# Performance work log

Hardware: AMD Instinct MI355X
Metric: run time of the kernel (lower is better)

## Reference

```python
import jax, jax.numpy as jnp
import numpy as np

N_EMBD = 1024
N_EXPERTS = 8
TOP_K = 2
D_FF = 4 * N_EMBD


def setup_inputs() -> dict:
    key = jax.random.key(0)
    ks = jax.random.split(key, 6)
    B, S = 4, 2048
    s = 1.0 / np.sqrt(N_EMBD)
    sf = 1.0 / np.sqrt(D_FF)
    x = jax.random.normal(ks[0], (B, S, N_EMBD), dtype=jnp.float32)
    router_w = jax.random.uniform(ks[1], (N_EMBD, N_EXPERTS), minval=-s, maxval=s, dtype=jnp.float32)
    wfc = jax.random.uniform(ks[2], (N_EXPERTS, N_EMBD, D_FF), minval=-s, maxval=s, dtype=jnp.float32)
    bfc = jax.random.uniform(ks[3], (N_EXPERTS, D_FF), minval=-s, maxval=s, dtype=jnp.float32)
    wproj = jax.random.uniform(ks[4], (N_EXPERTS, D_FF, N_EMBD), minval=-sf, maxval=sf, dtype=jnp.float32)
    bproj = jax.random.uniform(ks[5], (N_EXPERTS, N_EMBD), minval=-sf, maxval=sf, dtype=jnp.float32)
    return {"x": x, "router_w": router_w, "wfc": wfc, "bfc": bfc, "wproj": wproj, "bproj": bproj}


def reference(x, router_w, wfc, bfc, wproj, bproj):
    B, S, D = x.shape
    E = wfc.shape[0]
    xf = x.reshape(-1, D)  # [N, D] tokens
    logits = xf @ router_w  # [N, E]
    probs = jax.nn.softmax(logits.astype(jnp.float32), axis=-1)
    w, sel = jax.lax.top_k(probs, TOP_K)  # [N, K]
    w = w / jnp.sum(w, axis=-1, keepdims=True)  # norm_topk_prob
    w = w.astype(x.dtype)
    out = jnp.zeros_like(xf)
    for e in range(E):
        # per-token gate for expert e (0 if not routed here) -- same math as
        # gather -> MLP -> weighted scatter-add in the original
        gate = jnp.sum(jnp.where(sel == e, w, jnp.zeros_like(w)), axis=-1)  # [N]
        h = jax.nn.gelu(xf @ wfc[e] + bfc[e], approximate=False)  # [N, 4D]
        y = h @ wproj[e] + bproj[e]  # [N, D]
        out = out + gate[:, None] * y
    return out.reshape(B, S, D)
```

## Files before the change

### kernel.cpp

```cpp
#include <hip/hip_runtime.h>
#include <hip/hip_bf16.h>


#define N_TOK 8192
#define DMODEL 1024
#define NEXP 8
#define DFF 4096
#define CAP 8192
#define MAXW 136

typedef __attribute__((ext_vector_type(8))) short short8;
typedef __attribute__((ext_vector_type(4))) float f32x4;

#define GLOAD_LDS16(g, l)                                              \
  __builtin_amdgcn_global_load_lds(                                    \
      (const __attribute__((address_space(1))) unsigned int*)(g),      \
      (__attribute__((address_space(3))) unsigned int*)(l), 16, 0, 0)

__device__ __forceinline__ unsigned short f2bf(float f) {
  unsigned u = __float_as_uint(f);
  return (unsigned short)((u + 0x7FFFu + ((u >> 16) & 1u)) >> 16);
}

__device__ __forceinline__ float gelu_f(float v) {
  return 0.5f * v * (1.0f + erff(v * 0.70710678118654752f));
}

__global__ void router_k(const float* __restrict__ x, const float* __restrict__ rw,
                         int* __restrict__ cnt, int* __restrict__ tok,
                         float* __restrict__ gate, unsigned short* __restrict__ xb) {
  int lane = threadIdx.x & 63;
  int t = blockIdx.x * 4 + (threadIdx.x >> 6);
  const float* xr = x + (size_t)t * DMODEL;
  unsigned short* xbr = xb + (size_t)t * DMODEL;
  float p[8];
#pragma unroll
  for (int e = 0; e < 8; ++e) p[e] = 0.0f;
#pragma unroll
  for (int j = 0; j < DMODEL / 64; ++j) {
    int i = lane + j * 64;
    float xv = xr[i];
    xbr[i] = f2bf(xv);
    const float4* r = (const float4*)(rw + (size_t)i * 8);
    float4 a = r[0], b = r[1];
    p[0] += xv * a.x; p[1] += xv * a.y; p[2] += xv * a.z; p[3] += xv * a.w;
    p[4] += xv * b.x; p[5] += xv * b.y; p[6] += xv * b.z; p[7] += xv * b.w;
  }
#pragma unroll
  for (int e = 0; e < 8; ++e) {
#pragma unroll
    for (int off = 32; off; off >>= 1) p[e] += __shfl_xor(p[e], off, 64);
  }
  if (lane == 0) {
    int e1 = 0;
#pragma unroll
    for (int e = 1; e < 8; ++e) if (p[e] > p[e1]) e1 = e;
    int e2 = (e1 == 0) ? 1 : 0;
#pragma unroll
    for (int e = 0; e < 8; ++e) if (e != e1 && p[e] > p[e2]) e2 = e;
    float w1 = 1.0f / (1.0f + expf(p[e2] - p[e1]));
    float w2 = 1.0f - w1;
    int s1 = atomicAdd(&cnt[e1], 1);
    tok[e1 * CAP + s1] = t; gate[e1 * CAP + s1] = w1;
    int s2 = atomicAdd(&cnt[e2], 1);
    tok[e2 * CAP + s2] = t; gate[e2 * CAP + s2] = w2;
  }
}

__global__ void prefix_k(const int* __restrict__ cnt, int* __restrict__ off,
                         int* __restrict__ nwork, int* __restrict__ wl) {
  if (threadIdx.x == 0 && blockIdx.x == 0) {
    int s = 0, n = 0;
    for (int e = 0; e < NEXP; ++e) {
      off[e] = s;
      int ntile = (cnt[e] + 127) >> 7;
      for (int mt = 0; mt < ntile; ++mt) wl[n++] = (e << 16) | mt;
      s += cnt[e];
    }
    nwork[0] = n;
  }
}

__global__ __launch_bounds__(256) void cvt_wt_k(const float* __restrict__ W,
                                                unsigned short* __restrict__ WT,
                                                int K, int N) {
  __shared__ float ls[64][68];
  int b = blockIdx.x;
  int nkt = K >> 6, nnt = N >> 6;
  int kt = b % nkt;
  int nt = (b / nkt) % nnt;
  int e = b / (nkt * nnt);
  const float* Wb = W + (size_t)e * K * N + (size_t)(kt * 64) * N + nt * 64;
  int t = threadIdx.x;
  int nn = (t & 15) * 4, kr = t >> 4;
#pragma unroll
  for (int i = 0; i < 4; ++i) {
    float4 v = *(const float4*)(Wb + (size_t)(kr + 16 * i) * N + nn);
    *(float4*)&ls[kr + 16 * i][nn] = v;
  }
  __syncthreads();
  int on = t >> 2, kc = (t & 3) * 16;
  unsigned short* dst = WT + (size_t)e * N * K + (size_t)(nt * 64 + on) * K + kt * 64 + kc;
  short8 r0, r1;
#pragma unroll
  for (int j = 0; j < 8; ++j) r0[j] = (short)f2bf(ls[kc + j][on]);
#pragma unroll
  for (int j = 0; j < 8; ++j) r1[j] = (short)f2bf(ls[kc + 8 + j][on]);
  *(short8*)dst = r0;
  *(short8*)(dst + 8) = r1;
}

#define STAGE(buf, kk)                                                  \
  do {                                                                  \
    GLOAD_LDS16(gA + (kk), &As[buf][tid * 8]);                          \
    GLOAD_LDS16(gB + (kk), &Bs[buf][tid * 8]);                          \
    GLOAD_LDS16(gB2 + (kk), &Bs[buf][4096 + tid * 8]);                  \
  } while (0)

#define COMPUTE(buf)                                                            \
  do {                                                                          \
    short8 af[4], bfv[4];                                                       \
    _Pragma("unroll") for (int i = 0; i < 4; ++i)                               \
        af[i] = *(const short8*)&As[buf][(wr * 64 + i * 16 + fr) * 32 + co];    \
    _Pragma("unroll") for (int i = 0; i < 4; ++i)                               \
        bfv[i] = *(const short8*)&Bs[buf][(wc * 64 + i * 16 + fr) * 32 + co];   \
    _Pragma("unroll") for (int mi = 0; mi < 4; ++mi)                            \
        _Pragma("unroll") for (int ni = 0; ni < 4; ++ni)                        \
            acc[mi][ni] = __builtin_amdgcn_mfma_f32_16x16x32_bf16(              \
                af[mi], bfv[ni], acc[mi][ni], 0, 0, 0);                         \
  } while (0)

#define WAITV(n) asm volatile("s_waitcnt vmcnt(" #n ")" ::: "memory")
#define BAR() __builtin_amdgcn_s_barrier()

#define KLOOP(KTOT)                                                       \
  STAGE(0, 0);                                                            \
  STAGE(1, 32);                                                           \
  STAGE(2, 64);                                                           \
  {                                                                       \
    int k0 = 0;                                                           \
    _Pragma("unroll 1") for (int it = 0; it < ((KTOT) / 32 - 5) / 3; ++it) { \
      WAITV(6); BAR(); COMPUTE(0); BAR(); STAGE(0, k0 + 96);              \
      WAITV(6); BAR(); COMPUTE(1); BAR(); STAGE(1, k0 + 128);             \
      WAITV(6); BAR(); COMPUTE(2); BAR(); STAGE(2, k0 + 160);             \
      k0 += 96;                                                           \
    }                                                                     \
    WAITV(6); BAR(); COMPUTE(0); BAR(); STAGE(0, k0 + 96);                \
    WAITV(6); BAR(); COMPUTE(1); BAR(); STAGE(1, k0 + 128);               \
    WAITV(6); BAR(); COMPUTE(2);                                          \
    WAITV(3); BAR(); COMPUTE(0);                                          \
    WAITV(0); BAR(); COMPUTE(1);                                          \
  }

#define NT1 16
__global__ __launch_bounds__(512, 4) void gemm1a_k(
    const unsigned short* __restrict__ xb, const unsigned short* __restrict__ wT,
    const float* __restrict__ bfc, const int* __restrict__ cnt,
    const int* __restrict__ off, const int* __restrict__ tok,
    const int* __restrict__ nwork, const int* __restrict__ wl,
    unsigned short* __restrict__ h) {
  int bid = (int)(blockIdx.x & 7) * ((int)gridDim.x >> 3) + (int)(blockIdx.x >> 3);
  int widx = bid % MAXW;
  int nt = bid / MAXW;
  if (widx >= nwork[0]) return;
  int wle = wl[widx];
  int e = wle >> 16;
  int mt = wle & 0xffff;
  int Me = cnt[e];
  int base = off[e];
  int n0 = nt * 256;

  __shared__ __align__(16) unsigned short As[3][128 * 32];
  __shared__ __align__(16) unsigned short Bs[3][256 * 32];

  int tid = threadIdx.x;
  int lane = tid & 63, w = tid >> 6;
  int lc = (((tid & 3) ^ ((tid >> 2) & 3)) * 8);

  int ari = mt * 128 + (tid >> 2);
  int t0 = tok[e * CAP + ((ari < Me) ? ari : (Me - 1))];
  const unsigned short* gA = xb + (size_t)t0 * DMODEL + lc;
  const unsigned short* gB = wT + ((size_t)e * DFF + n0 + (tid >> 2)) * DMODEL + lc;
  const unsigned short* gB2 = gB + (size_t)128 * DMODEL;

  int wr = w >> 2, wc = w & 3;
  int g = lane >> 4, fr = lane & 15;
  int co = ((g ^ (fr & 3)) * 8);

  f32x4 acc[4][4];
#pragma unroll
  for (int i = 0; i < 4; ++i)
#pragma unroll
    for (int j = 0; j < 4; ++j) acc[i][j] = (f32x4)0.0f;

  KLOOP(DMODEL);

#pragma unroll
  for (int mi = 0; mi < 4; ++mi) {
    int rl = wr * 64 + mi * 16 + g * 4;
#pragma unroll
    for (int i = 0; i < 4; ++i) {
      int r = mt * 128 + rl + i;
      if (r < Me) {
        unsigned short* hrow = h + (size_t)(base + r) * DFF;
#pragma unroll
        for (int ni = 0; ni < 4; ++ni) {
          int col = n0 + wc * 64 + ni * 16 + fr;
          float v = acc[mi][ni][i] + bfc[e * DFF + col];
          hrow[col] = f2bf(gelu_f(v));
        }
      }
    }
  }
}

#define NT2 4
__global__ __launch_bounds__(512, 4) void gemm2a_k(
    const unsigned short* __restrict__ h, const unsigned short* __restrict__ wT,
    const float* __restrict__ bproj, const int* __restrict__ cnt,
    const int* __restrict__ off, const int* __restrict__ tok,
    const int* __restrict__ nwork, const int* __restrict__ wl,
    const float* __restrict__ gate, float* __restrict__ out) {
  int bid = (int)(blockIdx.x & 7) * ((int)gridDim.x >> 3) + (int)(blockIdx.x >> 3);
  int widx = bid % MAXW;
  int nt = bid / MAXW;
  if (widx >= nwork[0]) return;
  int wle = wl[widx];
  int e = wle >> 16;
  int mt = wle & 0xffff;
  int Me = cnt[e];
  int base = off[e];
  int n0 = nt * 256;

  __shared__ __align__(16) unsigned short As[3][128 * 32];
  __shared__ __align__(16) unsigned short Bs[3][256 * 32];

  int tid = threadIdx.x;
  int lane = tid & 63, w = tid >> 6;
  int lc = (((tid & 3) ^ ((tid >> 2) & 3)) * 8);

  const unsigned short* gA = h + (size_t)(base + mt * 128 + (tid >> 2)) * DFF + lc;
  const unsigned short* gB = wT + ((size_t)e * DMODEL + n0 + (tid >> 2)) * DFF + lc;
  const unsigned short* gB2 = gB + (size_t)128 * DFF;

  int wr = w >> 2, wc = w & 3;
  int g = lane >> 4, fr = lane & 15;
  int co = ((g ^ (fr & 3)) * 8);

  f32x4 acc[4][4];
#pragma unroll
  for (int i = 0; i < 4; ++i)
#pragma unroll
    for (int j = 0; j < 4; ++j) acc[i][j] = (f32x4)0.0f;

  KLOOP(DFF);

#pragma unroll
  for (int mi = 0; mi < 4; ++mi) {
    int rl = wr * 64 + mi * 16 + g * 4;
#pragma unroll
    for (int i = 0; i < 4; ++i) {
      int r = mt * 128 + rl + i;
      if (r < Me) {
        int tkn = tok[e * CAP + r];
        float gv = gate[e * CAP + r];
        float* orow = out + (size_t)tkn * DMODEL;
#pragma unroll
        for (int ni = 0; ni < 4; ++ni) {
          int col = n0 + wc * 64 + ni * 16 + fr;
          float v = acc[mi][ni][i] + bproj[e * DMODEL + col];
          atomicAdd(orow + col, gv * v);
        }
      }
    }
  }
}

extern "C" void kernel_launch(void* const* d_in, const int* in_sizes, int n_in,
                              void* d_out, int out_size, void* d_ws, size_t ws_size,
                              hipStream_t stream) {
  const float* x = (const float*)d_in[0];
  const float* rw = (const float*)d_in[1];
  const float* wfc = (const float*)d_in[2];
  const float* bfc = (const float*)d_in[3];
  const float* wproj = (const float*)d_in[4];
  const float* bproj = (const float*)d_in[5];
  float* out = (float*)d_out;

  char* ws = (char*)d_ws;
  int* cnt = (int*)ws;
  int* off_ = (int*)(ws + 64);
  int* nwork = (int*)(ws + 128);
  int* wl = (int*)(ws + 256);
  int* tok = (int*)(ws + 4096);
  float* gate = (float*)(ws + 4096 + (size_t)NEXP * CAP * 4);
  size_t HOFF = 4096 + 2 * (size_t)NEXP * CAP * 4;
  unsigned short* h = (unsigned short*)(ws + HOFF);
  size_t HSZ = (size_t)(16384 + 128) * DFF * 2;
  size_t XOFF = HOFF + HSZ;
  size_t WOFF = XOFF + (size_t)N_TOK * DMODEL * 2;
  size_t WSZ = (size_t)NEXP * DFF * DMODEL * 2;
  unsigned short* xb = (unsigned short*)(ws + XOFF);
  unsigned short* wT1 = (unsigned short*)(ws + WOFF);

  hipMemsetAsync(cnt, 0, 128, stream);
  hipMemsetAsync(out, 0, (size_t)out_size * 4, stream);
  router_k<<<N_TOK / 4, 256, 0, stream>>>(x, rw, cnt, tok, gate, xb);
  prefix_k<<<1, 64, 0, stream>>>(cnt, off_, nwork, wl);

  if (ws_size >= WOFF + 2 * WSZ) {
    unsigned short* wT2 = (unsigned short*)(ws + WOFF + WSZ);
    cvt_wt_k<<<NEXP * (DMODEL / 64) * (DFF / 64), 256, 0, stream>>>(wfc, wT1, DMODEL, DFF);
    cvt_wt_k<<<NEXP * (DFF / 64) * (DMODEL / 64), 256, 0, stream>>>(wproj, wT2, DFF, DMODEL);
    gemm1a_k<<<MAXW * NT1, 512, 0, stream>>>(xb, wT1, bfc, cnt, off_, tok, nwork, wl, h);
    gemm2a_k<<<MAXW * NT2, 512, 0, stream>>>(h, wT2, bproj, cnt, off_, tok, nwork, wl, gate, out);
  } else {
    cvt_wt_k<<<NEXP * (DMODEL / 64) * (DFF / 64), 256, 0, stream>>>(wfc, wT1, DMODEL, DFF);
    gemm1a_k<<<MAXW * NT1, 512, 0, stream>>>(xb, wT1, bfc, cnt, off_, tok, nwork, wl, h);
    cvt_wt_k<<<NEXP * (DFF / 64) * (DMODEL / 64), 256, 0, stream>>>(wproj, wT1, DFF, DMODEL);
    gemm2a_k<<<MAXW * NT2, 512, 0, stream>>>(h, wT1, bproj, cnt, off_, tok, nwork, wl, gate, out);
  }
}
```

Before: 815.0 us.

## Enlarge GEMM tiles to 256x256x64 with double-buffered LDS and setprio

```diff
diff --git a/kernel.cpp b/kernel.cpp
--- a/kernel.cpp
+++ b/kernel.cpp
@@ -7,7 +7,7 @@
 #define NEXP 8
 #define DFF 4096
 #define CAP 8192
-#define MAXW 136
+#define MAXW 72
 
 typedef __attribute__((ext_vector_type(8))) short short8;
 typedef __attribute__((ext_vector_type(4))) float f32x4;
@@ -73,7 +73,7 @@
     int s = 0, n = 0;
     for (int e = 0; e < NEXP; ++e) {
       off[e] = s;
-      int ntile = (cnt[e] + 127) >> 7;
+      int ntile = (cnt[e] + 255) >> 8;
       for (int mt = 0; mt < ntile; ++mt) wl[n++] = (e << 16) | mt;
       s += cnt[e];
     }
@@ -110,50 +110,52 @@
   *(short8*)(dst + 8) = r1;
 }
 
-#define STAGE(buf, kk)                                                  \
+#define STAGE(buf, kt)                                                  \
   do {                                                                  \
-    GLOAD_LDS16(gA + (kk), &As[buf][tid * 8]);                          \
-    GLOAD_LDS16(gB + (kk), &Bs[buf][tid * 8]);                          \
-    GLOAD_LDS16(gB2 + (kk), &Bs[buf][4096 + tid * 8]);                  \
+    int kk_ = (kt) * 64;                                                \
+    GLOAD_LDS16(gA0 + kk_, &As[buf][dL0]);                              \
+    GLOAD_LDS16(gA1 + kk_, &As[buf][dL1]);                              \
+    GLOAD_LDS16(gA2 + kk_, &As[buf][dL2]);                              \
+    GLOAD_LDS16(gA3 + kk_, &As[buf][dL3]);                              \
+    GLOAD_LDS16(gB0 + kk_, &Bs[buf][dL0]);                              \
+    GLOAD_LDS16(gB1 + kk_, &Bs[buf][dL1]);                              \
+    GLOAD_LDS16(gB2 + kk_, &Bs[buf][dL2]);                              \
+    GLOAD_LDS16(gB3 + kk_, &Bs[buf][dL3]);                              \
   } while (0)
 
-#define COMPUTE(buf)                                                            \
-  do {                                                                          \
-    short8 af[4], bfv[4];                                                       \
-    _Pragma("unroll") for (int i = 0; i < 4; ++i)                               \
-        af[i] = *(const short8*)&As[buf][(wr * 64 + i * 16 + fr) * 32 + co];    \
-    _Pragma("unroll") for (int i = 0; i < 4; ++i)                               \
-        bfv[i] = *(const short8*)&Bs[buf][(wc * 64 + i * 16 + fr) * 32 + co];   \
-    _Pragma("unroll") for (int mi = 0; mi < 4; ++mi)                            \
-        _Pragma("unroll") for (int ni = 0; ni < 4; ++ni)                        \
-            acc[mi][ni] = __builtin_amdgcn_mfma_f32_16x16x32_bf16(              \
-                af[mi], bfv[ni], acc[mi][ni], 0, 0, 0);                         \
+#define COMPUTE(buf)                                                             \
+  do {                                                                           \
+    __builtin_amdgcn_s_setprio(1);                                               \
+    _Pragma("unroll") for (int kk = 0; kk < 2; ++kk) {                           \
+      int co = kk ? co1 : co0;                                                   \
+      short8 af[8], bfv[4];                                                      \
+      _Pragma("unroll") for (int mi = 0; mi < 8; ++mi)                           \
+          af[mi] = *(const short8*)&As[buf][(wr * 128 + mi * 16 + fr) * 64 + co];\
+      _Pragma("unroll") for (int ni = 0; ni < 4; ++ni)                           \
+          bfv[ni] = *(const short8*)&Bs[buf][(wc * 64 + ni * 16 + fr) * 64 + co];\
+      _Pragma("unroll") for (int mi = 0; mi < 8; ++mi)                           \
+          _Pragma("unroll") for (int ni = 0; ni < 4; ++ni)                       \
+              acc[mi][ni] = __builtin_amdgcn_mfma_f32_16x16x32_bf16(             \
+                  af[mi], bfv[ni], acc[mi][ni], 0, 0, 0);                        \
+    }                                                                            \
+    __builtin_amdgcn_s_setprio(0);                                               \
   } while (0)
 
-#define WAITV(n) asm volatile("s_waitcnt vmcnt(" #n ")" ::: "memory")
+#define VMCNT0() asm volatile("s_waitcnt vmcnt(0)" ::: "memory")
 #define BAR() __builtin_amdgcn_s_barrier()
 
-#define KLOOP(KTOT)                                                       \
-  STAGE(0, 0);                                                            \
-  STAGE(1, 32);                                                           \
-  STAGE(2, 64);                                                           \
-  {                                                                       \
-    int k0 = 0;                                                           \
-    _Pragma("unroll 1") for (int it = 0; it < ((KTOT) / 32 - 5) / 3; ++it) { \
-      WAITV(6); BAR(); COMPUTE(0); BAR(); STAGE(0, k0 + 96);              \
-      WAITV(6); BAR(); COMPUTE(1); BAR(); STAGE(1, k0 + 128);             \
-      WAITV(6); BAR(); COMPUTE(2); BAR(); STAGE(2, k0 + 160);             \
-      k0 += 96;                                                           \
-    }                                                                     \
-    WAITV(6); BAR(); COMPUTE(0); BAR(); STAGE(0, k0 + 96);                \
-    WAITV(6); BAR(); COMPUTE(1); BAR(); STAGE(1, k0 + 128);               \
-    WAITV(6); BAR(); COMPUTE(2);                                          \
-    WAITV(3); BAR(); COMPUTE(0);                                          \
-    WAITV(0); BAR(); COMPUTE(1);                                          \
-  }
+#define KLOOP(NT_)                                                  \
+  STAGE(0, 0);                                                      \
+  VMCNT0(); BAR();                                                  \
+  _Pragma("unroll 1") for (int t = 0; t + 2 < (NT_); t += 2) {      \
+    STAGE(1, t + 1); COMPUTE(0); VMCNT0(); BAR();                   \
+    STAGE(0, t + 2); COMPUTE(1); VMCNT0(); BAR();                   \
+  }                                                                 \
+  STAGE(1, (NT_)-1); COMPUTE(0); VMCNT0(); BAR();                   \
+  COMPUTE(1);
 
 #define NT1 16
-__global__ __launch_bounds__(512, 4) void gemm1a_k(
+__global__ __launch_bounds__(512, 1) void gemm1a_k(
     const unsigned short* __restrict__ xb, const unsigned short* __restrict__ wT,
     const float* __restrict__ bfc, const int* __restrict__ cnt,
     const int* __restrict__ off, const int* __restrict__ tok,
@@ -170,37 +172,49 @@
   int base = off[e];
   int n0 = nt * 256;
 
-  __shared__ __align__(16) unsigned short As[3][128 * 32];
-  __shared__ __align__(16) unsigned short Bs[3][256 * 32];
+  __shared__ __align__(16) unsigned short As[2][256 * 64];
+  __shared__ __align__(16) unsigned short Bs[2][256 * 64];
 
   int tid = threadIdx.x;
   int lane = tid & 63, w = tid >> 6;
-  int lc = (((tid & 3) ^ ((tid >> 2) & 3)) * 8);
-
-  int ari = mt * 128 + (tid >> 2);
-  int t0 = tok[e * CAP + ((ari < Me) ? ari : (Me - 1))];
-  const unsigned short* gA = xb + (size_t)t0 * DMODEL + lc;
-  const unsigned short* gB = wT + ((size_t)e * DFF + n0 + (tid >> 2)) * DMODEL + lc;
-  const unsigned short* gB2 = gB + (size_t)128 * DMODEL;
+  int srow = tid >> 3;
+  int lcsw = (((tid & 7) ^ (srow & 7)) * 8);
+  int dL0 = srow * 64 + (tid & 7) * 8;
+  int dL1 = dL0 + 64 * 64, dL2 = dL0 + 128 * 64, dL3 = dL0 + 192 * 64;
+
+  int a0 = mt * 256 + srow;
+  int t0 = tok[e * CAP + ((a0 < Me) ? a0 : (Me - 1))];
+  int t1 = tok[e * CAP + ((a0 + 64 < Me) ? a0 + 64 : (Me - 1))];
+  int t2 = tok[e * CAP + ((a0 + 128 < Me) ? a0 + 128 : (Me - 1))];
+  int t3 = tok[e * CAP + ((a0 + 192 < Me) ? a0 + 192 : (Me - 1))];
+  const unsigned short* gA0 = xb + (size_t)t0 * DMODEL + lcsw;
+  const unsigned short* gA1 = xb + (size_t)t1 * DMODEL + lcsw;
+  const unsigned short* gA2 = xb + (size_t)t2 * DMODEL + lcsw;
+  const unsigned short* gA3 = xb + (size_t)t3 * DMODEL + lcsw;
+  const unsigned short* gB0 = wT + ((size_t)e * DFF + n0 + srow) * DMODEL + lcsw;
+  const unsigned short* gB1 = gB0 + (size_t)64 * DMODEL;
+  const unsigned short* gB2 = gB0 + (size_t)128 * DMODEL;
+  const unsigned short* gB3 = gB0 + (size_t)192 * DMODEL;
 
   int wr = w >> 2, wc = w & 3;
   int g = lane >> 4, fr = lane & 15;
-  int co = ((g ^ (fr & 3)) * 8);
-
-  f32x4 acc[4][4];
-#pragma unroll
-  for (int i = 0; i < 4; ++i)
+  int co0 = ((g ^ (fr & 7)) * 8);
+  int co1 = (((4 + g) ^ (fr & 7)) * 8);
+
+  f32x4 acc[8][4];
+#pragma unroll
+  for (int i = 0; i < 8; ++i)
 #pragma unroll
     for (int j = 0; j < 4; ++j) acc[i][j] = (f32x4)0.0f;
 
-  KLOOP(DMODEL);
-
-#pragma unroll
-  for (int mi = 0; mi < 4; ++mi) {
-    int rl = wr * 64 + mi * 16 + g * 4;
+  KLOOP(NT1);
+
+#pragma unroll
+  for (int mi = 0; mi < 8; ++mi) {
+    int rl = wr * 128 + mi * 16 + g * 4;
 #pragma unroll
     for (int i = 0; i < 4; ++i) {
-      int r = mt * 128 + rl + i;
+      int r = mt * 256 + rl + i;
       if (r < Me) {
         unsigned short* hrow = h + (size_t)(base + r) * DFF;
 #pragma unroll
@@ -215,7 +229,7 @@
 }
 
 #define NT2 4
-__global__ __launch_bounds__(512, 4) void gemm2a_k(
+__global__ __launch_bounds__(512, 1) void gemm2a_k(
     const unsigned short* __restrict__ h, const unsigned short* __restrict__ wT,
     const float* __restrict__ bproj, const int* __restrict__ cnt,
     const int* __restrict__ off, const int* __restrict__ tok,
@@ -232,35 +246,44 @@
   int base = off[e];
   int n0 = nt * 256;
 
-  __shared__ __align__(16) unsigned short As[3][128 * 32];
-  __shared__ __align__(16) unsigned short Bs[3][256 * 32];
+  __shared__ __align__(16) unsigned short As[2][256 * 64];
+  __shared__ __align__(16) unsigned short Bs[2][256 * 64];
 
   int tid = threadIdx.x;
   int lane = tid & 63, w = tid >> 6;
-  int lc = (((tid & 3) ^ ((tid >> 2) & 3)) * 8);
-
-  const unsigned short* gA = h + (size_t)(base + mt * 128 + (tid >> 2)) * DFF + lc;
-  const unsigned short* gB = wT + ((size_t)e * DMODEL + n0 + (tid >> 2)) * DFF + lc;
-  const unsigned short* gB2 = gB + (size_t)128 * DFF;
+  int srow = tid >> 3;
+  int lcsw = (((tid & 7) ^ (srow & 7)) * 8);
+  int dL0 = srow * 64 + (tid & 7) * 8;
+  int dL1 = dL0 + 64 * 64, dL2 = dL0 + 128 * 64, dL3 = dL0 + 192 * 64;
+
+  const unsigned short* gA0 = h + (size_t)(base + mt * 256 + srow) * DFF + lcsw;
+  const unsigned short* gA1 = gA0 + (size_t)64 * DFF;
+  const unsigned short* gA2 = gA0 + (size_t)128 * DFF;
+  const unsigned short* gA3 = gA0 + (size_t)192 * DFF;
+  const unsigned short* gB0 = wT + ((size_t)e * DMODEL + n0 + srow) * DFF + lcsw;
+  const unsigned short* gB1 = gB0 + (size_t)64 * DFF;
+  const unsigned short* gB2 = gB0 + (size_t)128 * DFF;
+  const unsigned short* gB3 = gB0 + (size_t)192 * DFF;
 
   int wr = w >> 2, wc = w & 3;
   int g = lane >> 4, fr = lane & 15;
-  int co = ((g ^ (fr & 3)) * 8);
-
-  f32x4 acc[4][4];
-#pragma unroll
-  for (int i = 0; i < 4; ++i)
+  int co0 = ((g ^ (fr & 7)) * 8);
+  int co1 = (((4 + g) ^ (fr & 7)) * 8);
+
+  f32x4 acc[8][4];
+#pragma unroll
+  for (int i = 0; i < 8; ++i)
 #pragma unroll
     for (int j = 0; j < 4; ++j) acc[i][j] = (f32x4)0.0f;
 
-  KLOOP(DFF);
-
-#pragma unroll
-  for (int mi = 0; mi < 4; ++mi) {
-    int rl = wr * 64 + mi * 16 + g * 4;
+  KLOOP(64);
+
+#pragma unroll
+  for (int mi = 0; mi < 8; ++mi) {
+    int rl = wr * 128 + mi * 16 + g * 4;
 #pragma unroll
     for (int i = 0; i < 4; ++i) {
-      int r = mt * 128 + rl + i;
+      int r = mt * 256 + rl + i;
       if (r < Me) {
         int tkn = tok[e * CAP + r];
         float gv = gate[e * CAP + r];
@@ -296,7 +319,7 @@
   float* gate = (float*)(ws + 4096 + (size_t)NEXP * CAP * 4);
   size_t HOFF = 4096 + 2 * (size_t)NEXP * CAP * 4;
   unsigned short* h = (unsigned short*)(ws + HOFF);
-  size_t HSZ = (size_t)(16384 + 128) * DFF * 2;
+  size_t HSZ = (size_t)(16384 + 256) * DFF * 2;
   size_t XOFF = HOFF + HSZ;
   size_t WOFF = XOFF + (size_t)N_TOK * DMODEL * 2;
   size_t WSZ = (size_t)NEXP * DFF * DMODEL * 2;
```

Measured after the change: 1.013 ms. +24.3%, slower.
